# Performance work log

Hardware: AMD Instinct MI355X
Metric: run time of the kernel (lower is better)

Reference implementation:

```python
import jax, jax.numpy as jnp
import numpy as np

B, T, D = 1, 1024, 2048
F_DIM = 1408
E = 8
TOPK = 2


def setup_inputs() -> dict:
    key = jax.random.key(0)
    ks = jax.random.split(key, 5)
    x = jax.random.normal(ks[0], (B, T, D), dtype=jnp.float32)
    # torch nn.Linear weight layout: [out_features, in_features]
    gate_w = jax.random.normal(ks[1], (E, D), dtype=jnp.float32) * 0.02
    gate_proj = jax.random.normal(ks[2], (E, F_DIM, D), dtype=jnp.float32) * 0.02
    up_proj = jax.random.normal(ks[3], (E, F_DIM, D), dtype=jnp.float32) * 0.02
    down_proj = jax.random.normal(ks[4], (E, D, F_DIM), dtype=jnp.float32) * 0.02
    return {"x": x, "gate_w": gate_w, "gate_proj": gate_proj,
            "up_proj": up_proj, "down_proj": down_proj}


def reference(x, gate_w, gate_proj, up_proj, down_proj):
    b, t, d = x.shape
    x_flat = x.reshape(-1, d)                                  # [N, D]
    n = x_flat.shape[0]
    # Router: top-k logits then softmax over the selected k.
    router_logits = x_flat @ gate_w.T                          # [N, E]
    top_w, sel = jax.lax.top_k(router_logits, TOPK)            # [N, K]
    top_w = jax.nn.softmax(top_w, axis=-1)                     # [N, K]
    # Scatter routing weights into dense per-token expert weights [N, E].
    tok_ids = jnp.arange(n)[:, None]
    tw = jnp.zeros((n, E), dtype=x.dtype).at[tok_ids, sel].add(top_w)
    # Dense expert compute (mathematically identical: unselected experts get
    # zero combine weight). SwiGLU per expert.
    g = jnp.einsum('nd,efd->enf', x_flat, gate_proj)           # [E, N, F]
    u = jnp.einsum('nd,efd->enf', x_flat, up_proj)             # [E, N, F]
    h = jax.nn.silu(g) * u                                     # [E, N, F]
    eo = jnp.einsum('enf,edf->end', h, down_proj)              # [E, N, D]
    out = jnp.einsum('end,ne->nd', eo, tw)                     # [N, D]
    return out.reshape(b, t, d)
```

## Files before the change

kernel.cpp:

```cpp
#include <hip/hip_runtime.h>
#include <hip/hip_bf16.h>
#include <stdint.h>

typedef __attribute__((ext_vector_type(8))) short short8;
typedef __attribute__((ext_vector_type(4))) float f32x4;
typedef unsigned int u32;
typedef unsigned short u16;

static constexpr int N_TOK = 1024;
static constexpr int DDIM = 2048;
static constexpr int FDIM = 1408;
static constexpr int NEXP = 8;
static constexpr int MAXROWS = 3072;
static constexpr int NT128 = 24;

static constexpr size_t O_META   = 0;
static constexpr size_t O_TE128  = 256;
static constexpr size_t O_TR128  = 384;
static constexpr size_t O_ROWTOK = 768;
static constexpr size_t O_TOKROWS= O_ROWTOK + (size_t)MAXROWS * 4;
static constexpr size_t O_SEL    = O_TOKROWS + 2048 * 4;
static constexpr size_t O_W      = O_SEL + 2048 * 4;
static constexpr size_t O_XBF    = (O_W + 2048 * 4 + 255) & ~(size_t)255;
static constexpr size_t O_H      = O_XBF + (size_t)(N_TOK + 1) * DDIM * 2;
static constexpr size_t O_WROW   = O_H + (size_t)MAXROWS * FDIM * 2;

static __device__ __forceinline__ u16 f2bf(float f) {
    return __builtin_bit_cast(u16, __float2bfloat16(f));
}
static __device__ __forceinline__ float bf2f(u16 s) {
    u32 u = ((u32)s) << 16;
    return __builtin_bit_cast(float, u);
}
static __device__ __forceinline__ u32 pack2(float a, float b) {
    return (u32)f2bf(a) | ((u32)f2bf(b) << 16);
}
static __device__ __forceinline__ void gload16(const void* g, void* l) {
    __builtin_amdgcn_global_load_lds(
        (const __attribute__((address_space(1))) void*)g,
        (__attribute__((address_space(3))) void*)l, 16, 0, 0);
}
#define PIN() __builtin_amdgcn_sched_barrier(0)
static __device__ __forceinline__ void sync_lgkm() {
    asm volatile("s_waitcnt lgkmcnt(0)" ::: "memory");
    __builtin_amdgcn_s_barrier();
    __builtin_amdgcn_sched_barrier(0);
}

__global__ __launch_bounds__(256) void zero_out_kernel(float* __restrict__ out)
{
    const long idx = ((long)blockIdx.x * 256 + threadIdx.x) * 4;
    *(float4*)(out + idx) = make_float4(0.f, 0.f, 0.f, 0.f);
}

__global__ __launch_bounds__(256) void router_kernel(
    const float* __restrict__ x, const float* __restrict__ gw,
    int* __restrict__ sel, float* __restrict__ wout, u16* __restrict__ xbf)
{
    __shared__ float xs[DDIM];
    __shared__ float lg[NEXP];
    const int tok = blockIdx.x;
    const float* xr = x + (size_t)tok * DDIM;
    for (int i = threadIdx.x; i < DDIM / 4; i += 256)
        ((float4*)xs)[i] = ((const float4*)xr)[i];
    __syncthreads();
    {
        const int i = threadIdx.x * 8;
        uint4 v;
        v.x = pack2(xs[i], xs[i + 1]);     v.y = pack2(xs[i + 2], xs[i + 3]);
        v.z = pack2(xs[i + 4], xs[i + 5]); v.w = pack2(xs[i + 6], xs[i + 7]);
        *(uint4*)(xbf + (size_t)tok * DDIM + i) = v;
        if (tok == 0)
            *(uint4*)(xbf + (size_t)N_TOK * DDIM + i) = uint4{0u, 0u, 0u, 0u};
    }
    const int wid = threadIdx.x >> 6, lane = threadIdx.x & 63;
    for (int i = 0; i < 2; i++) {
        const int e = wid * 2 + i;
        const float* g = gw + (size_t)e * DDIM;
        float s = 0.f;
        for (int k = lane; k < DDIM; k += 64) s += xs[k] * g[k];
        for (int off = 32; off > 0; off >>= 1) s += __shfl_down(s, off);
        if (lane == 0) lg[e] = s;
    }
    __syncthreads();
    if (threadIdx.x == 0) {
        int i1 = 0;
        for (int e = 1; e < NEXP; e++) if (lg[e] > lg[i1]) i1 = e;
        int i2 = -1;
        for (int e = 0; e < NEXP; e++) {
            if (e == i1) continue;
            if (i2 < 0 || lg[e] > lg[i2]) i2 = e;
        }
        const float e2 = __expf(lg[i2] - lg[i1]);
        const float w1 = 1.f / (1.f + e2);
        sel[tok * 2] = i1; sel[tok * 2 + 1] = i2;
        wout[tok * 2] = w1; wout[tok * 2 + 1] = e2 * w1;
    }
}

__global__ __launch_bounds__(512) void build_kernel(
    const int* __restrict__ sel, const float* __restrict__ w,
    int* __restrict__ meta, int* __restrict__ te128, int* __restrict__ tr128,
    int* __restrict__ row_tok, int* __restrict__ tok_rows, float* __restrict__ wrow)
{
    __shared__ int s0[N_TOK], s1[N_TOK];
    __shared__ u16 p0[N_TOK], p1[N_TOK];
    __shared__ int counts[NEXP], offs[NEXP];
    for (int i = threadIdx.x; i < N_TOK; i += 512) {
        s0[i] = sel[i * 2]; s1[i] = sel[i * 2 + 1];
    }
    __syncthreads();
    const int e = threadIdx.x >> 6, lane = threadIdx.x & 63;
    int base = 0;
    for (int c = 0; c < N_TOK / 64; c++) {
        const int tk = c * 64 + lane;
        const int slot = (s0[tk] == e) ? 0 : ((s1[tk] == e) ? 1 : -1);
        const unsigned long long m = __ballot(slot >= 0);
        const int pre = __popcll(m & ((1ull << lane) - 1ull));
        if (slot == 0) p0[tk] = (u16)(base + pre);
        else if (slot == 1) p1[tk] = (u16)(base + pre);
        base += __popcll(m);
    }
    if (lane == 0) counts[e] = base;
    __syncthreads();
    if (threadIdx.x == 0) {
        int off = 0, n128 = 0;
        for (int qq = 0; qq < NEXP; qq++) {
            offs[qq] = off;
            const int pc = (counts[qq] + 127) & ~127;
            for (int i = 0; i < pc / 128; i++) { te128[n128] = qq; tr128[n128] = off + i * 128; n128++; }
            off += pc;
        }
        meta[0] = n128; meta[1] = off;
    }
    __syncthreads();
    const int off = offs[e];
    for (int c = 0; c < N_TOK / 64; c++) {
        const int tk = c * 64 + lane;
        const int slot = (s0[tk] == e) ? 0 : ((s1[tk] == e) ? 1 : -1);
        if (slot >= 0) {
            const int row = off + (slot ? p1[tk] : p0[tk]);
            row_tok[row] = tk;
            tok_rows[tk * 2 + slot] = row;
            wrow[row] = w[tk * 2 + slot];
        }
    }
    const int cnt = counts[e];
    const int pc = (cnt + 127) & ~127;
    for (int p = cnt + lane; p < pc; p += 64) { row_tok[off + p] = -1; wrow[off + p] = 0.f; }
}

__global__ __launch_bounds__(512, 4) void mlp1_kernel(
    const u16* __restrict__ xbf,
    const float* __restrict__ gp, const float* __restrict__ upw,
    u16* __restrict__ h,
    const int* __restrict__ meta, const int* __restrict__ te128,
    const int* __restrict__ tr128, const int* __restrict__ row_tok,
    const float* __restrict__ wrow)
{
    const int tile = blockIdx.y;
    const int nb = blockIdx.x;
    if (tile >= meta[0]) return;
    const int n0 = nb * 32;
    const int e = te128[tile];
    const int r0g = tr128[tile];

    __shared__ __align__(16) u16 As[2][128 * 64];
    __shared__ __align__(16) u16 Bs0[2][32 * 64];
    __shared__ __align__(16) u16 Bs1[2][32 * 64];

    const int t = threadIdx.x;
    const int wid = t >> 6, lane = t & 63;
    const int lr = lane & 15, lhi = lane >> 4;

    const u16* asrc[2];
    int aldsoff[2];
    #pragma unroll
    for (int j = 0; j < 2; j++) {
        const int row = wid * 16 + j * 8 + (lane >> 3);
        const int gran = (lane & 7) ^ (row & 7);
        const int tok = row_tok[r0g + row];
        asrc[j] = xbf + (size_t)(tok < 0 ? N_TOK : tok) * DDIM + gran * 8;
        aldsoff[j] = (wid * 2 + j) * 512;
    }

    const int rb = t >> 4, c4 = t & 15;
    const float* brow0 = gp  + (size_t)e * FDIM * DDIM + (size_t)(n0 + rb) * DDIM + c4 * 4;
    const float* brow1 = upw + (size_t)e * FDIM * DDIM + (size_t)(n0 + rb) * DDIM + c4 * 4;
    const int sOffB = rb * 64 + (((c4 >> 1) ^ (rb & 7)) * 8) + (c4 & 1) * 4;

    const int wm = wid * 16;

    f32x4 acc0[2], acc1[2];
    acc0[0] = acc0[1] = acc1[0] = acc1[1] = f32x4{0.f, 0.f, 0.f, 0.f};
    float4 pb0P, pb1P, pb0Q, pb1Q;

    auto STAGEA = [&](int bsel, int k0) {
        #pragma unroll
        for (int j = 0; j < 2; j++)
            gload16(asrc[j] + k0, &As[bsel][aldsoff[j]]);
    };
    auto LOADB_P = [&](int k0) {
        pb0P = *(const float4*)(brow0 + k0);
        pb1P = *(const float4*)(brow1 + k0);
    };
    auto LOADB_Q = [&](int k0) {
        pb0Q = *(const float4*)(brow0 + k0);
        pb1Q = *(const float4*)(brow1 + k0);
    };
    auto STOREB_P = [&](int bsel) {
        uint2 v0; v0.x = pack2(pb0P.x, pb0P.y); v0.y = pack2(pb0P.z, pb0P.w);
        *(uint2*)(&Bs0[bsel][sOffB]) = v0;
        uint2 v1; v1.x = pack2(pb1P.x, pb1P.y); v1.y = pack2(pb1P.z, pb1P.w);
        *(uint2*)(&Bs1[bsel][sOffB]) = v1;
    };
    auto STOREB_Q = [&](int bsel) {
        uint2 v0; v0.x = pack2(pb0Q.x, pb0Q.y); v0.y = pack2(pb0Q.z, pb0Q.w);
        *(uint2*)(&Bs0[bsel][sOffB]) = v0;
        uint2 v1; v1.x = pack2(pb1Q.x, pb1Q.y); v1.y = pack2(pb1Q.z, pb1Q.w);
        *(uint2*)(&Bs1[bsel][sOffB]) = v1;
    };
    auto COMPUTE = [&](int bsel) {
        __builtin_amdgcn_s_setprio(1);
        #pragma unroll
        for (int ks = 0; ks < 2; ks++) {
            short8 a, b0[2], b1[2];
            {
                const int rowa = wm + lr;
                const int gr = (ks * 4 + lhi) ^ (rowa & 7);
                a = *(const short8*)(&As[bsel][rowa * 64 + gr * 8]);
            }
            #pragma unroll
            for (int n = 0; n < 2; n++) {
                const int rowb = n * 16 + lr;
                const int gr = (ks * 4 + lhi) ^ (rowb & 7);
                b0[n] = *(const short8*)(&Bs0[bsel][rowb * 64 + gr * 8]);
                b1[n] = *(const short8*)(&Bs1[bsel][rowb * 64 + gr * 8]);
            }
            #pragma unroll
            for (int n = 0; n < 2; n++) {
                acc0[n] = __builtin_amdgcn_mfma_f32_16x16x32_bf16(a, b0[n], acc0[n], 0, 0, 0);
                acc1[n] = __builtin_amdgcn_mfma_f32_16x16x32_bf16(a, b1[n], acc1[n], 0, 0, 0);
            }
        }
        __builtin_amdgcn_s_setprio(0);
    };

    constexpr int NT = DDIM / 64;
    STAGEA(0, 0);
    PIN();
    LOADB_P(0);
    LOADB_Q(64);
    PIN();
    STOREB_P(0);
    sync_lgkm();
    for (int kt = 0; kt < NT; kt += 2) {
        STAGEA(1, ((kt + 1) & (NT - 1)) * 64);
        PIN();
        LOADB_P(((kt + 2) & (NT - 1)) * 64);
        PIN();
        STOREB_Q(1);
        asm volatile("s_waitcnt vmcnt(4)" ::: "memory");
        PIN();
        COMPUTE(0);
        sync_lgkm();
        STAGEA(0, ((kt + 2) & (NT - 1)) * 64);
        PIN();
        LOADB_Q(((kt + 3) & (NT - 1)) * 64);
        PIN();
        STOREB_P(0);
        asm volatile("s_waitcnt vmcnt(4)" ::: "memory");
        PIN();
        COMPUTE(1);
        sync_lgkm();
    }

    #pragma unroll
    for (int j = 0; j < 4; j++) {
        const int row = r0g + wm + lhi * 4 + j;
        const float wr = wrow[row];
        #pragma unroll
        for (int n = 0; n < 2; n++) {
            const int col = n0 + n * 16 + lr;
            const float g = acc0[n][j], u = acc1[n][j];
            const float hv = g / (1.f + __expf(-g)) * u * wr;
            h[(size_t)row * FDIM + col] = f2bf(hv);
        }
    }
}

__global__ __launch_bounds__(512, 6) void down_kernel(
    const u16* __restrict__ h, const float* __restrict__ dp,
    float* __restrict__ out,
    const int* __restrict__ meta, const int* __restrict__ te128,
    const int* __restrict__ tr128, const int* __restrict__ row_tok)
{
    const int tile = blockIdx.y;
    const int nb = blockIdx.x;
    if (tile >= meta[0]) return;
    const int n0 = nb * 64;
    const int e = te128[tile];
    const int r0g = tr128[tile];

    __shared__ __align__(16) u16 As[2][128 * 64];
    __shared__ __align__(16) u16 Bs[2][64 * 64];

    const int t = threadIdx.x;
    const int wid = t >> 6, lane = t & 63;
    const int lr = lane & 15, lhi = lane >> 4;

    const u16* asrc[2];
    int aldsoff[2];
    #pragma unroll
    for (int j = 0; j < 2; j++) {
        const int row = wid * 16 + j * 8 + (lane >> 3);
        const int gran = (lane & 7) ^ (row & 7);
        asrc[j] = h + (size_t)(r0g + row) * FDIM + gran * 8;
        aldsoff[j] = (wid * 2 + j) * 512;
    }

    const int rb = t >> 3, g8 = t & 7;
    const float* brow = dp + (size_t)e * DDIM * FDIM + (size_t)(n0 + rb) * FDIM + g8 * 8;
    const int sOffB = rb * 64 + ((g8 ^ (rb & 7)) * 8);

    const int wm = wid * 16;

    f32x4 acc[4];
    #pragma unroll
    for (int n = 0; n < 4; n++) acc[n] = f32x4{0.f,0.f,0.f,0.f};
    float4 paP, pbP, paQ, pbQ;

    auto STAGEA = [&](int bsel, int k0) {
        #pragma unroll
        for (int j = 0; j < 2; j++)
            gload16(asrc[j] + k0, &As[bsel][aldsoff[j]]);
    };
    auto LOADB_P = [&](int k0) {
        paP = *(const float4*)(brow + k0); pbP = *(const float4*)(brow + k0 + 4);
    };
    auto LOADB_Q = [&](int k0) {
        paQ = *(const float4*)(brow + k0); pbQ = *(const float4*)(brow + k0 + 4);
    };
    auto STOREB_P = [&](int bsel) {
        uint4 v; v.x = pack2(paP.x, paP.y); v.y = pack2(paP.z, paP.w);
        v.z = pack2(pbP.x, pbP.y); v.w = pack2(pbP.z, pbP.w);
        *(uint4*)(&Bs[bsel][sOffB]) = v;
    };
    auto STOREB_Q = [&](int bsel) {
        uint4 v; v.x = pack2(paQ.x, paQ.y); v.y = pack2(paQ.z, paQ.w);
        v.z = pack2(pbQ.x, pbQ.y); v.w = pack2(pbQ.z, pbQ.w);
        *(uint4*)(&Bs[bsel][sOffB]) = v;
    };
    auto COMPUTE = [&](int bsel) {
        __builtin_amdgcn_s_setprio(1);
        #pragma unroll
        for (int ks = 0; ks < 2; ks++) {
            short8 a;
            {
                const int rowa = wm + lr;
                const int gr = (ks * 4 + lhi) ^ (rowa & 7);
                a = *(const short8*)(&As[bsel][rowa * 64 + gr * 8]);
            }
            #pragma unroll
            for (int n = 0; n < 4; n++) {
                const int rowb = n * 16 + lr;
                const int gr = (ks * 4 + lhi) ^ (rowb & 7);
                const short8 b = *(const short8*)(&Bs[bsel][rowb * 64 + gr * 8]);
                acc[n] = __builtin_amdgcn_mfma_f32_16x16x32_bf16(a, b, acc[n], 0, 0, 0);
            }
        }
        __builtin_amdgcn_s_setprio(0);
    };

    constexpr int NT = FDIM / 64;
    STAGEA(0, 0);
    PIN();
    LOADB_P(0);
    LOADB_Q(64);
    PIN();
    STOREB_P(0);
    sync_lgkm();
    for (int kt = 0; kt < NT; kt += 2) {
        int k1 = kt + 1; if (k1 >= NT) k1 = 0;
        int k2 = kt + 2; if (k2 >= NT) k2 = 0;
        int k3 = kt + 3; if (k3 >= NT) k3 = 0;
        STAGEA(1, k1 * 64);
        PIN();
        LOADB_P(k2 * 64);
        PIN();
        STOREB_Q(1);
        asm volatile("s_waitcnt vmcnt(4)" ::: "memory");
        PIN();
        COMPUTE(0);
        sync_lgkm();
        STAGEA(0, k2 * 64);
        PIN();
        LOADB_Q(k3 * 64);
        PIN();
        STOREB_P(0);
        asm volatile("s_waitcnt vmcnt(4)" ::: "memory");
        PIN();
        COMPUTE(1);
        sync_lgkm();
    }

    #pragma unroll
    for (int j = 0; j < 4; j++) {
        const int row = r0g + wm + lhi * 4 + j;
        const int tok = row_tok[row];
        if (tok >= 0) {
            float* orow = out + (size_t)tok * DDIM;
            #pragma unroll
            for (int n = 0; n < 4; n++) {
                const int col = n0 + n * 16 + lr;
                atomicAdd(orow + col, acc[n][j]);
            }
        }
    }
}

extern "C" void kernel_launch(void* const* d_in, const int* in_sizes, int n_in,
                              void* d_out, int out_size, void* d_ws, size_t ws_size,
                              hipStream_t stream) {
    const float* x  = (const float*)d_in[0];
    const float* gw = (const float*)d_in[1];
    const float* gp = (const float*)d_in[2];
    const float* up = (const float*)d_in[3];
    const float* dp = (const float*)d_in[4];
    float* out = (float*)d_out;
    char* ws = (char*)d_ws;

    int*   meta     = (int*)(ws + O_META);
    int*   te128    = (int*)(ws + O_TE128);
    int*   tr128    = (int*)(ws + O_TR128);
    int*   row_tok  = (int*)(ws + O_ROWTOK);
    int*   tok_rows = (int*)(ws + O_TOKROWS);
    int*   sel      = (int*)(ws + O_SEL);
    float* w        = (float*)(ws + O_W);
    u16*   xbf      = (u16*)(ws + O_XBF);
    u16*   h        = (u16*)(ws + O_H);
    float* wrow     = (float*)(ws + O_WROW);

    zero_out_kernel<<<(N_TOK * DDIM) / (256 * 4), 256, 0, stream>>>(out);
    router_kernel<<<N_TOK, 256, 0, stream>>>(x, gw, sel, w, xbf);
    build_kernel<<<1, 512, 0, stream>>>(sel, w, meta, te128, tr128,
                                        row_tok, tok_rows, wrow);
    mlp1_kernel<<<dim3(FDIM / 32, NT128), 512, 0, stream>>>(
        xbf, gp, up, h, meta, te128, tr128, row_tok, wrow);
    down_kernel<<<dim3(DDIM / 64, NT128), 512, 0, stream>>>(
        h, dp, out, meta, te128, tr128, row_tok);
}
```

Measured before the change: 184.5 us.

## Replace atomic scatter-add with bf16 expert-output buffer and per-token combine kernel

The down projection now writes bf16 per-row expert outputs to a workspace buffer instead of atomically adding fp32 results into the output, and a new combine kernel gathers each token's two rows and applies the routing weights. This removes the output zeroing kernel and the fp32 atomics on global memory, and moves the routing-weight multiply out of the mlp1 epilogue. In exchange it adds an extra launch, a round trip of a 3072x2048 bf16 buffer through memory, and extra bf16 rounding of the expert outputs before weighting.

```diff
diff --git a/kernel.cpp b/kernel.cpp
--- a/kernel.cpp
+++ b/kernel.cpp
@@ -23,7 +23,7 @@
 static constexpr size_t O_W      = O_SEL + 2048 * 4;
 static constexpr size_t O_XBF    = (O_W + 2048 * 4 + 255) & ~(size_t)255;
 static constexpr size_t O_H      = O_XBF + (size_t)(N_TOK + 1) * DDIM * 2;
-static constexpr size_t O_WROW   = O_H + (size_t)MAXROWS * FDIM * 2;
+static constexpr size_t O_EO     = O_H + (size_t)MAXROWS * FDIM * 2;
 
 static __device__ __forceinline__ u16 f2bf(float f) {
     return __builtin_bit_cast(u16, __float2bfloat16(f));
@@ -45,12 +45,6 @@
     asm volatile("s_waitcnt lgkmcnt(0)" ::: "memory");
     __builtin_amdgcn_s_barrier();
     __builtin_amdgcn_sched_barrier(0);
-}
-
-__global__ __launch_bounds__(256) void zero_out_kernel(float* __restrict__ out)
-{
-    const long idx = ((long)blockIdx.x * 256 + threadIdx.x) * 4;
-    *(float4*)(out + idx) = make_float4(0.f, 0.f, 0.f, 0.f);
 }
 
 __global__ __launch_bounds__(256) void router_kernel(
@@ -99,9 +93,9 @@
 }
 
 __global__ __launch_bounds__(512) void build_kernel(
-    const int* __restrict__ sel, const float* __restrict__ w,
+    const int* __restrict__ sel,
     int* __restrict__ meta, int* __restrict__ te128, int* __restrict__ tr128,
-    int* __restrict__ row_tok, int* __restrict__ tok_rows, float* __restrict__ wrow)
+    int* __restrict__ row_tok, int* __restrict__ tok_rows)
 {
     __shared__ int s0[N_TOK], s1[N_TOK];
     __shared__ u16 p0[N_TOK], p1[N_TOK];
@@ -142,12 +136,11 @@
             const int row = off + (slot ? p1[tk] : p0[tk]);
             row_tok[row] = tk;
             tok_rows[tk * 2 + slot] = row;
-            wrow[row] = w[tk * 2 + slot];
         }
     }
     const int cnt = counts[e];
     const int pc = (cnt + 127) & ~127;
-    for (int p = cnt + lane; p < pc; p += 64) { row_tok[off + p] = -1; wrow[off + p] = 0.f; }
+    for (int p = cnt + lane; p < pc; p += 64) row_tok[off + p] = -1;
 }
 
 __global__ __launch_bounds__(512, 4) void mlp1_kernel(
@@ -155,8 +148,7 @@
     const float* __restrict__ gp, const float* __restrict__ upw,
     u16* __restrict__ h,
     const int* __restrict__ meta, const int* __restrict__ te128,
-    const int* __restrict__ tr128, const int* __restrict__ row_tok,
-    const float* __restrict__ wrow)
+    const int* __restrict__ tr128, const int* __restrict__ row_tok)
 {
     const int tile = blockIdx.y;
     const int nb = blockIdx.x;
@@ -276,14 +268,13 @@
     }
 
     #pragma unroll
-    for (int j = 0; j < 4; j++) {
-        const int row = r0g + wm + lhi * 4 + j;
-        const float wr = wrow[row];
-        #pragma unroll
-        for (int n = 0; n < 2; n++) {
-            const int col = n0 + n * 16 + lr;
+    for (int n = 0; n < 2; n++) {
+        const int col = n0 + n * 16 + lr;
+        #pragma unroll
+        for (int j = 0; j < 4; j++) {
+            const int row = r0g + wm + lhi * 4 + j;
             const float g = acc0[n][j], u = acc1[n][j];
-            const float hv = g / (1.f + __expf(-g)) * u * wr;
+            const float hv = g / (1.f + __expf(-g)) * u;
             h[(size_t)row * FDIM + col] = f2bf(hv);
         }
     }
@@ -291,9 +282,9 @@
 
 __global__ __launch_bounds__(512, 6) void down_kernel(
     const u16* __restrict__ h, const float* __restrict__ dp,
-    float* __restrict__ out,
+    u16* __restrict__ eo,
     const int* __restrict__ meta, const int* __restrict__ te128,
-    const int* __restrict__ tr128, const int* __restrict__ row_tok)
+    const int* __restrict__ tr128)
 {
     const int tile = blockIdx.y;
     const int nb = blockIdx.x;
@@ -405,18 +396,37 @@
     }
 
     #pragma unroll
-    for (int j = 0; j < 4; j++) {
-        const int row = r0g + wm + lhi * 4 + j;
-        const int tok = row_tok[row];
-        if (tok >= 0) {
-            float* orow = out + (size_t)tok * DDIM;
-            #pragma unroll
-            for (int n = 0; n < 4; n++) {
-                const int col = n0 + n * 16 + lr;
-                atomicAdd(orow + col, acc[n][j]);
-            }
-        }
-    }
+    for (int n = 0; n < 4; n++) {
+        const int col = n0 + n * 16 + lr;
+        #pragma unroll
+        for (int j = 0; j < 4; j++) {
+            const int row = r0g + wm + lhi * 4 + j;
+            eo[(size_t)row * DDIM + col] = f2bf(acc[n][j]);
+        }
+    }
+}
+
+__global__ __launch_bounds__(256) void combine_kernel(
+    const u16* __restrict__ eo, const int* __restrict__ tok_rows,
+    const float* __restrict__ w, float* __restrict__ out)
+{
+    const int tok = blockIdx.x;
+    const int r1 = tok_rows[tok * 2], r2 = tok_rows[tok * 2 + 1];
+    const float w1 = w[tok * 2], w2 = w[tok * 2 + 1];
+    const int d = threadIdx.x * 8;
+    const uint4 a = *(const uint4*)(eo + (size_t)r1 * DDIM + d);
+    const uint4 b = *(const uint4*)(eo + (size_t)r2 * DDIM + d);
+    const u32 av[4] = {a.x, a.y, a.z, a.w};
+    const u32 bv[4] = {b.x, b.y, b.z, b.w};
+    float4 o0, o1;
+    float* op[8] = {&o0.x, &o0.y, &o0.z, &o0.w, &o1.x, &o1.y, &o1.z, &o1.w};
+    #pragma unroll
+    for (int i = 0; i < 4; i++) {
+        *op[2 * i]     = w1 * bf2f((u16)(av[i] & 0xffff)) + w2 * bf2f((u16)(bv[i] & 0xffff));
+        *op[2 * i + 1] = w1 * bf2f((u16)(av[i] >> 16))    + w2 * bf2f((u16)(bv[i] >> 16));
+    }
+    float4* po = (float4*)(out + (size_t)tok * DDIM + d);
+    po[0] = o0; po[1] = o1;
 }
 
 extern "C" void kernel_launch(void* const* d_in, const int* in_sizes, int n_in,
@@ -439,14 +449,13 @@
     float* w        = (float*)(ws + O_W);
     u16*   xbf      = (u16*)(ws + O_XBF);
     u16*   h        = (u16*)(ws + O_H);
-    float* wrow     = (float*)(ws + O_WROW);
-
-    zero_out_kernel<<<(N_TOK * DDIM) / (256 * 4), 256, 0, stream>>>(out);
+    u16*   eo       = (u16*)(ws + O_EO);
+
     router_kernel<<<N_TOK, 256, 0, stream>>>(x, gw, sel, w, xbf);
-    build_kernel<<<1, 512, 0, stream>>>(sel, w, meta, te128, tr128,
-                                        row_tok, tok_rows, wrow);
+    build_kernel<<<1, 512, 0, stream>>>(sel, meta, te128, tr128, row_tok, tok_rows);
     mlp1_kernel<<<dim3(FDIM / 32, NT128), 512, 0, stream>>>(
-        xbf, gp, up, h, meta, te128, tr128, row_tok, wrow);
+        xbf, gp, up, h, meta, te128, tr128, row_tok);
     down_kernel<<<dim3(DDIM / 64, NT128), 512, 0, stream>>>(
-        h, dp, out, meta, te128, tr128, row_tok);
-}
+        h, dp, eo, meta, te128, tr128);
+    combine_kernel<<<N_TOK, 256, 0, stream>>>(eo, tok_rows, w, out);
+}
```

New measurement: 178.5 us. -3.2%, faster.
